# Kernel tuning notes

Measured on AMD Instinct MI355X. Metric: run time of the kernel, lower is better.

The kernel has to match this reference:

```python
import jax, jax.numpy as jnp
import numpy as np

N, C_IN, C_OUT, H, RANK = 16, 4, 32, 400, 4


def setup_inputs() -> dict:
    key = jax.random.key(0)
    k1, k2, k3 = jax.random.split(key, 3)
    x = jax.random.normal(k1, (N, C_IN, H, H), dtype=jnp.float32)
    # symmetric sylo: weight_R tied to weight_L (shape C_out x C_in x H x rank)
    fan_in = C_IN * H
    scale = 1.0 / np.sqrt(fan_in)
    weight_L = jax.random.normal(k2, (C_OUT, C_IN, H, RANK), dtype=jnp.float32) * scale
    bias = jax.random.uniform(k3, (C_OUT,), dtype=jnp.float32, minval=-scale, maxval=scale)
    return {"x": x, "weight_L": weight_L, "bias": bias}


def reference(x, weight_L, bias):
    # Expand low-rank symmetric template: T[o,c] = L[o,c] @ L[o,c].T  (H x H)
    T = jnp.einsum('ocir,ocjr->ocij', weight_L, weight_L)
    # Crosshair similarity, summed over input channels:
    # out[n,o,i,j] = sum_c [ sum_k X[n,c,i,k]T[o,c,i,k] + sum_k X[n,c,k,j]T[o,c,k,j] - X[n,c,i,j]T[o,c,i,j] ]
    rows = jnp.einsum('ncik,ocik->noi', x, T)   # row sums of X*T
    cols = jnp.einsum('nckj,ockj->noj', x, T)   # column sums of X*T
    diag = jnp.einsum('ncij,ocij->noij', x, T)  # pointwise term (counted twice)
    out = rows[..., :, None] + cols[..., None, :] - diag
    return out + bias[None, :, None, None]
```

## Files before the change

kernel.cpp:

```cpp
#include <hip/hip_runtime.h>

#define H  400
#define NB 16
#define CI 4
#define CO 32

#define TT 80
__global__ __launch_bounds__(256) void k_transpose(const float* __restrict__ x,
                                                   float* __restrict__ xt) {
    __shared__ float tile[TT][TT + 5];
    int b = blockIdx.x;
    int tj = b % 5;
    int ti = (b / 5) % 5;
    int nc = b / 25;
    const float* src = x + (size_t)nc * H * H;
    float* dst = xt + (size_t)nc * H * H;
    int i0 = ti * TT, j0 = tj * TT;
    for (int e = threadIdx.x; e < TT * 20; e += 256) {
        int r = e / 20, q = e % 20;
        float4 v = ((const float4*)(src + (size_t)(i0 + r) * H + j0))[q];
        tile[r][q * 4 + 0] = v.x; tile[r][q * 4 + 1] = v.y;
        tile[r][q * 4 + 2] = v.z; tile[r][q * 4 + 3] = v.w;
    }
    __syncthreads();
    for (int e = threadIdx.x; e < TT * 20; e += 256) {
        int r = e / 20, q = e % 20;
        float4 v;
        v.x = tile[q * 4 + 0][r]; v.y = tile[q * 4 + 1][r];
        v.z = tile[q * 4 + 2][r]; v.w = tile[q * 4 + 3][r];
        ((float4*)(dst + (size_t)(j0 + r) * H + i0))[q] = v;
    }
}

#define KC 40
#define KSPLIT 5
__global__ __launch_bounds__(256) void k_rowscols(const float* __restrict__ x,
        const float* __restrict__ xt, const float* __restrict__ L,
        float* __restrict__ rowsP, float* __restrict__ colsP)
{
    __shared__ __align__(16) float4 Lm[CO * CI];
    __shared__ __align__(16) float Xr[NB * CI * KC];
    __shared__ __align__(16) float Xc[NB * CI * KC];
    __shared__ __align__(16) float Tr[CO * 164];
    int b = blockIdx.x;
    int m  = b / KSPLIT;
    int ks = b % KSPLIT;
    int tid = threadIdx.x;
    const float4* L4 = (const float4*)L;
    if (tid < CO * CI) Lm[tid] = L4[tid * H + m];

    int o  = tid & 31;
    int n0 = tid >> 5;
    float ar0 = 0.f, ar1 = 0.f, ac0 = 0.f, ac1 = 0.f;

    for (int ch = 0; ch < 2; ++ch) {
        int k0 = ks * 80 + ch * KC;
        __syncthreads();
        for (int e = tid; e < NB * CI * KC / 4; e += 256) {
            int q  = e % 10;
            int nc = e / 10;
            ((float4*)Xr)[e] = *(const float4*)(x  + (size_t)(nc * H + m) * H + k0 + q * 4);
            ((float4*)Xc)[e] = *(const float4*)(xt + (size_t)(nc * H + m) * H + k0 + q * 4);
        }
        for (int e = tid; e < CO * CI * KC; e += 256) {
            int k  = e % KC;
            int oc = e / KC;
            float4 lv = L4[oc * H + k0 + k];
            float4 lm = Lm[oc];
            Tr[(oc >> 2) * 164 + (oc & 3) * KC + k] =
                lv.x * lm.x + lv.y * lm.y + lv.z * lm.z + lv.w * lm.w;
        }
        __syncthreads();
        #pragma unroll
        for (int c = 0; c < CI; ++c) {
            const float4* trp = (const float4*)(Tr + o * 164 + c * KC);
            const float4* pr0 = (const float4*)(Xr + (n0 * CI + c) * KC);
            const float4* pr1 = (const float4*)(Xr + ((n0 + 8) * CI + c) * KC);
            const float4* pc0 = (const float4*)(Xc + (n0 * CI + c) * KC);
            const float4* pc1 = (const float4*)(Xc + ((n0 + 8) * CI + c) * KC);
            #pragma unroll
            for (int q = 0; q < KC / 4; ++q) {
                float4 tv = trp[q];
                float4 a  = pr0[q];
                float4 bb = pr1[q];
                float4 cc = pc0[q];
                float4 dd = pc1[q];
                ar0 += tv.x * a.x  + tv.y * a.y  + tv.z * a.z  + tv.w * a.w;
                ar1 += tv.x * bb.x + tv.y * bb.y + tv.z * bb.z + tv.w * bb.w;
                ac0 += tv.x * cc.x + tv.y * cc.y + tv.z * cc.z + tv.w * cc.w;
                ac1 += tv.x * dd.x + tv.y * dd.y + tv.z * dd.z + tv.w * dd.w;
            }
        }
    }
    size_t base = ((size_t)ks * H + m) * (NB * CO);
    rowsP[base + tid]       = ar0;
    rowsP[base + 256 + tid] = ar1;
    colsP[base + tid]       = ac0;
    colsP[base + 256 + tid] = ac1;
}

__global__ __launch_bounds__(256) void k_reduce(const float* __restrict__ rowsP,
        const float* __restrict__ colsP, float* __restrict__ rows, float* __restrict__ cols)
{
    int i = blockIdx.x * 256 + threadIdx.x;
    int m  = i % H;
    int no = i / H;
    float s = 0.f, t = 0.f;
    #pragma unroll
    for (int k = 0; k < KSPLIT; ++k) {
        s += rowsP[((size_t)k * H + m) * (NB * CO) + no];
        t += colsP[((size_t)k * H + m) * (NB * CO) + no];
    }
    rows[(size_t)no * H + m] = s;
    cols[(size_t)no * H + m] = t;
}

#define TS 16
__global__ __launch_bounds__(256, 4) void k_out(const float* __restrict__ x,
        const float* __restrict__ L, const float* __restrict__ bias,
        const float* __restrict__ rows, const float* __restrict__ cols,
        float* __restrict__ out)
{
    __shared__ __align__(16) float Xl[8 * CI * TS * TS];
    __shared__ __align__(16) float rT[8 * 4 * TS];
    __shared__ __align__(16) float cT[8 * 4 * TS];
    int b = blockIdx.x;
    int ti = b / 25, tj = b % 25;
    int i0 = ti * TS, j0 = tj * TS;
    int tid = threadIdx.x;

    int o  = tid >> 6;
    int u  = tid & 63;
    int ii = u >> 2, jq = u & 3;
    const float4* x4  = (const float4*)x;
    const float4* L4  = (const float4*)L;
    const float4* cT4 = (const float4*)cT;
    float4* Xl4  = (float4*)Xl;
    float4* out4 = (float4*)out;

    for (int nh = 0; nh < 2; ++nh) {
        if (nh) __syncthreads();
        for (int e = tid; e < 8 * CI * TS * 4; e += 256) {
            int q   = e & 3;
            int iiw = (e >> 2) & 15;
            int nc  = nh * (8 * CI) + (e >> 6);
            Xl4[e] = x4[(size_t)(nc * H + i0 + iiw) * 100 + tj * 4 + q];
        }
        for (int os = 0; os < 8; ++os) {
            int og = os * 4 + o;
            float4 T4[CI];
            #pragma unroll
            for (int c = 0; c < CI; ++c) {
                float4 Li = L4[(og * CI + c) * H + i0 + ii];
                float4 La = L4[(og * CI + c) * H + j0 + jq * 4 + 0];
                float4 Lb = L4[(og * CI + c) * H + j0 + jq * 4 + 1];
                float4 Lc = L4[(og * CI + c) * H + j0 + jq * 4 + 2];
                float4 Ld = L4[(og * CI + c) * H + j0 + jq * 4 + 3];
                T4[c].x = Li.x * La.x + Li.y * La.y + Li.z * La.z + Li.w * La.w;
                T4[c].y = Li.x * Lb.x + Li.y * Lb.y + Li.z * Lb.z + Li.w * Lb.w;
                T4[c].z = Li.x * Lc.x + Li.y * Lc.y + Li.z * Lc.z + Li.w * Lc.w;
                T4[c].w = Li.x * Ld.x + Li.y * Ld.y + Li.z * Ld.z + Li.w * Ld.w;
            }
            float bo = bias[og];

            __syncthreads();
            for (int e = tid; e < 8 * 4 * TS; e += 256) {
                int iw = e & 15;
                int oo = (e >> 4) & 3;
                int np = e >> 6;
                int n  = nh * 8 + np;
                rT[e] = rows[(size_t)(n * CO + os * 4 + oo) * H + i0 + iw];
                cT[e] = cols[(size_t)(n * CO + os * 4 + oo) * H + j0 + iw];
            }
            __syncthreads();

            for (int np = 0; np < 8; ++np) {
                float ra  = rT[(np * 4 + o) * TS + ii] + bo;
                float4 ca = cT4[(np * 4 + o) * 4 + jq];
                float4 acc;
                acc.x = ra + ca.x; acc.y = ra + ca.y; acc.z = ra + ca.z; acc.w = ra + ca.w;
                #pragma unroll
                for (int c = 0; c < CI; ++c) {
                    float4 xv = Xl4[((np * CI + c) * TS + ii) * 4 + jq];
                    acc.x -= xv.x * T4[c].x;
                    acc.y -= xv.y * T4[c].y;
                    acc.z -= xv.z * T4[c].z;
                    acc.w -= xv.w * T4[c].w;
                }
                int n = nh * 8 + np;
                out4[((size_t)(n * CO + og) * H + i0 + ii) * 100 + tj * 4 + jq] = acc;
            }
        }
    }
}

extern "C" void kernel_launch(void* const* d_in, const int* in_sizes, int n_in,
                              void* d_out, int out_size, void* d_ws, size_t ws_size,
                              hipStream_t stream) {
    const float* x    = (const float*)d_in[0];
    const float* L    = (const float*)d_in[1];
    const float* bias = (const float*)d_in[2];
    float* out = (float*)d_out;
    char* ws = (char*)d_ws;

    size_t xt_bytes = (size_t)NB * CI * H * H * sizeof(float);
    size_t rc_elems = (size_t)NB * CO * H;
    size_t rcP_bytes = (size_t)KSPLIT * rc_elems * sizeof(float);
    size_t rc_bytes  = rc_elems * sizeof(float);

    float* XT    = (float*)ws;
    float* rowsP = (float*)(ws + xt_bytes);
    float* colsP = (float*)(ws + xt_bytes + rcP_bytes);
    float* rows  = (float*)(ws + xt_bytes + 2 * rcP_bytes);
    float* cols  = (float*)(ws + xt_bytes + 2 * rcP_bytes + rc_bytes);
    (void)ws_size;

    k_transpose<<<1600, 256, 0, stream>>>(x, XT);
    k_rowscols<<<H * KSPLIT, 256, 0, stream>>>(x, XT, L, rowsP, colsP);
    k_reduce<<<(NB * CO * H) / 256, 256, 0, stream>>>(rowsP, colsP, rows, cols);
    k_out<<<625, 256, 0, stream>>>(x, L, bias, rows, cols, out);
}
```

Before: 504.0 us.

## Compute row and column sums from shared 2D tiles, dropping the transpose pass

Removes the separate transpose kernel and the transposed copy of x. A new kernel computes row and column partial sums together from 16x16 tiles of x and T held in shared memory, so each x element is read once for both reductions. The partial sums and reduced rows/cols now use an i-major layout, which gives coalesced reads in the output kernel. The cost is 25 split partials instead of 5, so the reduce kernel reads much more data, and per-thread register arrays of 64 accumulators may limit occupancy.

```diff
diff --git a/kernel.cpp b/kernel.cpp
--- a/kernel.cpp
+++ b/kernel.cpp
@@ -4,121 +4,103 @@
 #define NB 16
 #define CI 4
 #define CO 32
-
-#define TT 80
-__global__ __launch_bounds__(256) void k_transpose(const float* __restrict__ x,
-                                                   float* __restrict__ xt) {
-    __shared__ float tile[TT][TT + 5];
-    int b = blockIdx.x;
-    int tj = b % 5;
-    int ti = (b / 5) % 5;
-    int nc = b / 25;
-    const float* src = x + (size_t)nc * H * H;
-    float* dst = xt + (size_t)nc * H * H;
-    int i0 = ti * TT, j0 = tj * TT;
-    for (int e = threadIdx.x; e < TT * 20; e += 256) {
-        int r = e / 20, q = e % 20;
-        float4 v = ((const float4*)(src + (size_t)(i0 + r) * H + j0))[q];
-        tile[r][q * 4 + 0] = v.x; tile[r][q * 4 + 1] = v.y;
-        tile[r][q * 4 + 2] = v.z; tile[r][q * 4 + 3] = v.w;
-    }
-    __syncthreads();
-    for (int e = threadIdx.x; e < TT * 20; e += 256) {
-        int r = e / 20, q = e % 20;
-        float4 v;
-        v.x = tile[q * 4 + 0][r]; v.y = tile[q * 4 + 1][r];
-        v.z = tile[q * 4 + 2][r]; v.w = tile[q * 4 + 3][r];
-        ((float4*)(dst + (size_t)(j0 + r) * H + i0))[q] = v;
-    }
-}
-
-#define KC 40
-#define KSPLIT 5
-__global__ __launch_bounds__(256) void k_rowscols(const float* __restrict__ x,
-        const float* __restrict__ xt, const float* __restrict__ L,
+#define NO (NB * CO)
+#define NS 25
+
+__global__ __launch_bounds__(256, 3) void k_rc(const float* __restrict__ x,
+        const float* __restrict__ L,
         float* __restrict__ rowsP, float* __restrict__ colsP)
 {
-    __shared__ __align__(16) float4 Lm[CO * CI];
-    __shared__ __align__(16) float Xr[NB * CI * KC];
-    __shared__ __align__(16) float Xc[NB * CI * KC];
-    __shared__ __align__(16) float Tr[CO * 164];
-    int b = blockIdx.x;
-    int m  = b / KSPLIT;
-    int ks = b % KSPLIT;
+    __shared__ __align__(16) float Xs[NB][16][16];
+    __shared__ __align__(16) float Ts[64][128];
+    int b  = blockIdx.x;
+    int ti = b / NS, tk = b % NS;
+    int I = ti * 16, K = tk * 16;
     int tid = threadIdx.x;
+    int o  = tid & 31;
+    int n2 = tid >> 5;
+    const float4* x4 = (const float4*)x;
     const float4* L4 = (const float4*)L;
-    if (tid < CO * CI) Lm[tid] = L4[tid * H + m];
-
-    int o  = tid & 31;
-    int n0 = tid >> 5;
-    float ar0 = 0.f, ar1 = 0.f, ac0 = 0.f, ac1 = 0.f;
-
-    for (int ch = 0; ch < 2; ++ch) {
-        int k0 = ks * 80 + ch * KC;
+
+    float ar0[16] = {}, ar1[16] = {}, ac0[16] = {}, ac1[16] = {};
+
+    for (int c = 0; c < CI; ++c) {
         __syncthreads();
-        for (int e = tid; e < NB * CI * KC / 4; e += 256) {
-            int q  = e % 10;
-            int nc = e / 10;
-            ((float4*)Xr)[e] = *(const float4*)(x  + (size_t)(nc * H + m) * H + k0 + q * 4);
-            ((float4*)Xc)[e] = *(const float4*)(xt + (size_t)(nc * H + m) * H + k0 + q * 4);
-        }
-        for (int e = tid; e < CO * CI * KC; e += 256) {
-            int k  = e % KC;
-            int oc = e / KC;
-            float4 lv = L4[oc * H + k0 + k];
-            float4 lm = Lm[oc];
-            Tr[(oc >> 2) * 164 + (oc & 3) * KC + k] =
-                lv.x * lm.x + lv.y * lm.y + lv.z * lm.z + lv.w * lm.w;
+        for (int e = tid; e < 1024; e += 256) {
+            int q  = e & 3;
+            int di = (e >> 2) & 15;
+            int n  = e >> 6;
+            ((float4*)Xs)[e] = x4[((size_t)(n * CI + c) * H + I + di) * 100 + tk * 4 + q];
+        }
+        {
+            const float4* Lrow = L4 + (size_t)(o * CI + c) * H;
+            float4 Li0 = Lrow[I + 2 * n2];
+            float4 Li1 = Lrow[I + 2 * n2 + 1];
+            #pragma unroll
+            for (int qk = 0; qk < 4; ++qk) {
+                float4 t0, t1;
+                #pragma unroll
+                for (int w = 0; w < 4; ++w) {
+                    float4 Lk = Lrow[K + qk * 4 + w];
+                    ((float*)&t0)[w] = Li0.x * Lk.x + Li0.y * Lk.y + Li0.z * Lk.z + Li0.w * Lk.w;
+                    ((float*)&t1)[w] = Li1.x * Lk.x + Li1.y * Lk.y + Li1.z * Lk.z + Li1.w * Lk.w;
+                }
+                *(float4*)&Ts[(2 * n2)     * 4 + qk][o * 4] = t0;
+                *(float4*)&Ts[(2 * n2 + 1) * 4 + qk][o * 4] = t1;
+            }
         }
         __syncthreads();
         #pragma unroll
-        for (int c = 0; c < CI; ++c) {
-            const float4* trp = (const float4*)(Tr + o * 164 + c * KC);
-            const float4* pr0 = (const float4*)(Xr + (n0 * CI + c) * KC);
-            const float4* pr1 = (const float4*)(Xr + ((n0 + 8) * CI + c) * KC);
-            const float4* pc0 = (const float4*)(Xc + (n0 * CI + c) * KC);
-            const float4* pc1 = (const float4*)(Xc + ((n0 + 8) * CI + c) * KC);
+        for (int di = 0; di < 16; ++di) {
             #pragma unroll
-            for (int q = 0; q < KC / 4; ++q) {
-                float4 tv = trp[q];
-                float4 a  = pr0[q];
-                float4 bb = pr1[q];
-                float4 cc = pc0[q];
-                float4 dd = pc1[q];
-                ar0 += tv.x * a.x  + tv.y * a.y  + tv.z * a.z  + tv.w * a.w;
-                ar1 += tv.x * bb.x + tv.y * bb.y + tv.z * bb.z + tv.w * bb.w;
-                ac0 += tv.x * cc.x + tv.y * cc.y + tv.z * cc.z + tv.w * cc.w;
-                ac1 += tv.x * dd.x + tv.y * dd.y + tv.z * dd.z + tv.w * dd.w;
-            }
-        }
-    }
-    size_t base = ((size_t)ks * H + m) * (NB * CO);
-    rowsP[base + tid]       = ar0;
-    rowsP[base + 256 + tid] = ar1;
-    colsP[base + tid]       = ac0;
-    colsP[base + 256 + tid] = ac1;
+            for (int qk = 0; qk < 4; ++qk) {
+                float4 tv = *(const float4*)&Ts[di * 4 + qk][o * 4];
+                float4 xa = ((const float4*)&Xs[n2][di][0])[qk];
+                float4 xb = ((const float4*)&Xs[n2 + 8][di][0])[qk];
+                ar0[di] += tv.x * xa.x + tv.y * xa.y + tv.z * xa.z + tv.w * xa.w;
+                ar1[di] += tv.x * xb.x + tv.y * xb.y + tv.z * xb.z + tv.w * xb.w;
+                ac0[qk * 4 + 0] += tv.x * xa.x;
+                ac0[qk * 4 + 1] += tv.y * xa.y;
+                ac0[qk * 4 + 2] += tv.z * xa.z;
+                ac0[qk * 4 + 3] += tv.w * xa.w;
+                ac1[qk * 4 + 0] += tv.x * xb.x;
+                ac1[qk * 4 + 1] += tv.y * xb.y;
+                ac1[qk * 4 + 2] += tv.z * xb.z;
+                ac1[qk * 4 + 3] += tv.w * xb.w;
+            }
+        }
+    }
+    int no0 = n2 * CO + o;
+    int no1 = (n2 + 8) * CO + o;
+    #pragma unroll
+    for (int d = 0; d < 16; ++d) {
+        rowsP[((size_t)tk * H + I + d) * NO + no0] = ar0[d];
+        rowsP[((size_t)tk * H + I + d) * NO + no1] = ar1[d];
+        colsP[((size_t)ti * H + K + d) * NO + no0] = ac0[d];
+        colsP[((size_t)ti * H + K + d) * NO + no1] = ac1[d];
+    }
 }
 
 __global__ __launch_bounds__(256) void k_reduce(const float* __restrict__ rowsP,
-        const float* __restrict__ colsP, float* __restrict__ rows, float* __restrict__ cols)
+        const float* __restrict__ colsP, float* __restrict__ rows2, float* __restrict__ cols2)
 {
-    int i = blockIdx.x * 256 + threadIdx.x;
-    int m  = i % H;
-    int no = i / H;
+    int idx = blockIdx.x * 256 + threadIdx.x;
+    int no = idx & (NO - 1);
+    int i  = idx >> 9;
     float s = 0.f, t = 0.f;
     #pragma unroll
-    for (int k = 0; k < KSPLIT; ++k) {
-        s += rowsP[((size_t)k * H + m) * (NB * CO) + no];
-        t += colsP[((size_t)k * H + m) * (NB * CO) + no];
-    }
-    rows[(size_t)no * H + m] = s;
-    cols[(size_t)no * H + m] = t;
+    for (int k = 0; k < NS; ++k) {
+        s += rowsP[((size_t)k * H + i) * NO + no];
+        t += colsP[((size_t)k * H + i) * NO + no];
+    }
+    rows2[(size_t)i * NO + no] = s;
+    cols2[(size_t)i * NO + no] = t;
 }
 
 #define TS 16
 __global__ __launch_bounds__(256, 4) void k_out(const float* __restrict__ x,
         const float* __restrict__ L, const float* __restrict__ bias,
-        const float* __restrict__ rows, const float* __restrict__ cols,
+        const float* __restrict__ rows2, const float* __restrict__ cols2,
         float* __restrict__ out)
 {
     __shared__ __align__(16) float Xl[8 * CI * TS * TS];
@@ -169,8 +151,8 @@
                 int oo = (e >> 4) & 3;
                 int np = e >> 6;
                 int n  = nh * 8 + np;
-                rT[e] = rows[(size_t)(n * CO + os * 4 + oo) * H + i0 + iw];
-                cT[e] = cols[(size_t)(n * CO + os * 4 + oo) * H + j0 + iw];
+                rT[e] = rows2[(size_t)(i0 + iw) * NO + n * CO + os * 4 + oo];
+                cT[e] = cols2[(size_t)(j0 + iw) * NO + n * CO + os * 4 + oo];
             }
             __syncthreads();
 
@@ -203,20 +185,16 @@
     float* out = (float*)d_out;
     char* ws = (char*)d_ws;
 
-    size_t xt_bytes = (size_t)NB * CI * H * H * sizeof(float);
-    size_t rc_elems = (size_t)NB * CO * H;
-    size_t rcP_bytes = (size_t)KSPLIT * rc_elems * sizeof(float);
-    size_t rc_bytes  = rc_elems * sizeof(float);
-
-    float* XT    = (float*)ws;
-    float* rowsP = (float*)(ws + xt_bytes);
-    float* colsP = (float*)(ws + xt_bytes + rcP_bytes);
-    float* rows  = (float*)(ws + xt_bytes + 2 * rcP_bytes);
-    float* cols  = (float*)(ws + xt_bytes + 2 * rcP_bytes + rc_bytes);
+    size_t rcP_bytes = (size_t)NS * H * NO * sizeof(float);
+    size_t rc_bytes  = (size_t)H * NO * sizeof(float);
+
+    float* rowsP = (float*)ws;
+    float* colsP = (float*)(ws + rcP_bytes);
+    float* rows2 = (float*)(ws + 2 * rcP_bytes);
+    float* cols2 = (float*)(ws + 2 * rcP_bytes + rc_bytes);
     (void)ws_size;
 
-    k_transpose<<<1600, 256, 0, stream>>>(x, XT);
-    k_rowscols<<<H * KSPLIT, 256, 0, stream>>>(x, XT, L, rowsP, colsP);
-    k_reduce<<<(NB * CO * H) / 256, 256, 0, stream>>>(rowsP, colsP, rows, cols);
-    k_out<<<625, 256, 0, stream>>>(x, L, bias, rows, cols, out);
-}
+    k_rc<<<NS * NS, 256, 0, stream>>>(x, L, rowsP, colsP);
+    k_reduce<<<(H * NO) / 256, 256, 0, stream>>>(rowsP, colsP, rows2, cols2);
+    k_out<<<625, 256, 0, stream>>>(x, L, bias, rows2, cols2, out);
+}
```

Result: slower. 644.2 us (+27.8%).

## Restructure output kernel to share template tiles in LDS and keep X in registers

Applied to the files above, without the earlier changes.

k_reduce now writes rows and cols in an m-major layout, so its reads and writes are coalesced and k_out's gathers read contiguous runs across n and o. In k_out each thread now owns one (n, i) row of a 16x16 tile and keeps its X values for all channels in registers. The T tile for four output channels is built once per block in shared memory from staged L rows, instead of each thread recomputing it from global L loads. The cost is more registers per thread (64 floats of X plus 16 accumulators) and extra barriers per output-channel group, which may lower occupancy.

```diff
diff --git a/kernel.cpp b/kernel.cpp
--- a/kernel.cpp
+++ b/kernel.cpp
@@ -4,6 +4,7 @@
 #define NB 16
 #define CI 4
 #define CO 32
+#define NO (NB * CO)
 
 #define TT 80
 __global__ __launch_bounds__(256) void k_transpose(const float* __restrict__ x,
@@ -92,7 +93,7 @@
             }
         }
     }
-    size_t base = ((size_t)ks * H + m) * (NB * CO);
+    size_t base = ((size_t)ks * H + m) * NO;
     rowsP[base + tid]       = ar0;
     rowsP[base + 256 + tid] = ar1;
     colsP[base + tid]       = ac0;
@@ -100,96 +101,113 @@
 }
 
 __global__ __launch_bounds__(256) void k_reduce(const float* __restrict__ rowsP,
-        const float* __restrict__ colsP, float* __restrict__ rows, float* __restrict__ cols)
+        const float* __restrict__ colsP, float* __restrict__ rows2, float* __restrict__ cols2)
 {
-    int i = blockIdx.x * 256 + threadIdx.x;
-    int m  = i % H;
-    int no = i / H;
+    int idx = blockIdx.x * 256 + threadIdx.x;
+    int no = idx & (NO - 1);
+    int m  = idx >> 9;
     float s = 0.f, t = 0.f;
     #pragma unroll
     for (int k = 0; k < KSPLIT; ++k) {
-        s += rowsP[((size_t)k * H + m) * (NB * CO) + no];
-        t += colsP[((size_t)k * H + m) * (NB * CO) + no];
-    }
-    rows[(size_t)no * H + m] = s;
-    cols[(size_t)no * H + m] = t;
-}
-
-#define TS 16
+        s += rowsP[((size_t)k * H + m) * NO + no];
+        t += colsP[((size_t)k * H + m) * NO + no];
+    }
+    rows2[(size_t)m * NO + no] = s;
+    cols2[(size_t)m * NO + no] = t;
+}
+
+#define TSP 20
+#define TS_OG (CI * 16 * TSP)
 __global__ __launch_bounds__(256, 4) void k_out(const float* __restrict__ x,
         const float* __restrict__ L, const float* __restrict__ bias,
-        const float* __restrict__ rows, const float* __restrict__ cols,
+        const float* __restrict__ rows2, const float* __restrict__ cols2,
         float* __restrict__ out)
 {
-    __shared__ __align__(16) float Xl[8 * CI * TS * TS];
-    __shared__ __align__(16) float rT[8 * 4 * TS];
-    __shared__ __align__(16) float cT[8 * 4 * TS];
+    __shared__ __align__(16) float4 Lsi[4 * CI * 16];
+    __shared__ __align__(16) float4 Lsj[4 * CI * 16];
+    __shared__ __align__(16) float  Ts[4 * TS_OG];
+    __shared__ __align__(16) float  rT[4 * NB * 16];
+    __shared__ __align__(16) float  cT[4 * NB * 16];
     int b = blockIdx.x;
     int ti = b / 25, tj = b % 25;
-    int i0 = ti * TS, j0 = tj * TS;
+    int i0 = ti * 16, j0 = tj * 16;
     int tid = threadIdx.x;
-
-    int o  = tid >> 6;
-    int u  = tid & 63;
-    int ii = u >> 2, jq = u & 3;
+    int n  = tid >> 4;
+    int ii = tid & 15;
     const float4* x4  = (const float4*)x;
     const float4* L4  = (const float4*)L;
     const float4* cT4 = (const float4*)cT;
-    float4* Xl4  = (float4*)Xl;
     float4* out4 = (float4*)out;
 
-    for (int nh = 0; nh < 2; ++nh) {
-        if (nh) __syncthreads();
-        for (int e = tid; e < 8 * CI * TS * 4; e += 256) {
-            int q   = e & 3;
-            int iiw = (e >> 2) & 15;
-            int nc  = nh * (8 * CI) + (e >> 6);
-            Xl4[e] = x4[(size_t)(nc * H + i0 + iiw) * 100 + tj * 4 + q];
-        }
-        for (int os = 0; os < 8; ++os) {
-            int og = os * 4 + o;
-            float4 T4[CI];
+    float4 Xr[CI][4];
+    #pragma unroll
+    for (int c = 0; c < CI; ++c)
+        #pragma unroll
+        for (int q = 0; q < 4; ++q)
+            Xr[c][q] = x4[((size_t)(n * CI + c) * H + i0 + ii) * 100 + tj * 4 + q];
+
+    for (int os = 0; os < 8; ++os) {
+        __syncthreads();
+        {
+            int r   = tid & 15;
+            int cg  = (tid >> 4) & 3;
+            int og_ = tid >> 6;
+            size_t lrow = (size_t)((os * 4 + og_) * CI + cg) * H;
+            Lsi[(og_ * CI + cg) * 16 + r] = L4[lrow + i0 + r];
+            Lsj[(og_ * CI + cg) * 16 + r] = L4[lrow + j0 + r];
+        }
+        for (int e = tid; e < 1024; e += 256) {
+            int iw  = e & 15;
+            int og_ = (e >> 4) & 3;
+            int nn  = e >> 6;
+            rT[(og_ * NB + nn) * 16 + iw] = rows2[(size_t)(i0 + iw) * NO + nn * CO + os * 4 + og_];
+            cT[(og_ * NB + nn) * 16 + iw] = cols2[(size_t)(j0 + iw) * NO + nn * CO + os * 4 + og_];
+        }
+        __syncthreads();
+        {
+            int iw  = tid & 15;
+            int cc  = (tid >> 4) & 3;
+            int og_ = tid >> 6;
+            float4 Li = Lsi[(og_ * CI + cc) * 16 + iw];
+            float* tsrow = Ts + og_ * TS_OG + cc * (16 * TSP) + iw * TSP;
+            #pragma unroll
+            for (int q = 0; q < 4; ++q) {
+                float4 t;
+                #pragma unroll
+                for (int w = 0; w < 4; ++w) {
+                    float4 Lj = Lsj[(og_ * CI + cc) * 16 + q * 4 + w];
+                    ((float*)&t)[w] = Li.x * Lj.x + Li.y * Lj.y + Li.z * Lj.z + Li.w * Lj.w;
+                }
+                *(float4*)(tsrow + q * 4) = t;
+            }
+        }
+        __syncthreads();
+        #pragma unroll
+        for (int og_ = 0; og_ < 4; ++og_) {
+            int og = os * 4 + og_;
+            float ra = rT[(og_ * NB + n) * 16 + ii] + bias[og];
+            float4 acc[4];
+            #pragma unroll
+            for (int q = 0; q < 4; ++q) {
+                float4 ca = cT4[(og_ * NB + n) * 4 + q];
+                acc[q].x = ra + ca.x; acc[q].y = ra + ca.y;
+                acc[q].z = ra + ca.z; acc[q].w = ra + ca.w;
+            }
             #pragma unroll
             for (int c = 0; c < CI; ++c) {
-                float4 Li = L4[(og * CI + c) * H + i0 + ii];
-                float4 La = L4[(og * CI + c) * H + j0 + jq * 4 + 0];
-                float4 Lb = L4[(og * CI + c) * H + j0 + jq * 4 + 1];
-                float4 Lc = L4[(og * CI + c) * H + j0 + jq * 4 + 2];
-                float4 Ld = L4[(og * CI + c) * H + j0 + jq * 4 + 3];
-                T4[c].x = Li.x * La.x + Li.y * La.y + Li.z * La.z + Li.w * La.w;
-                T4[c].y = Li.x * Lb.x + Li.y * Lb.y + Li.z * Lb.z + Li.w * Lb.w;
-                T4[c].z = Li.x * Lc.x + Li.y * Lc.y + Li.z * Lc.z + Li.w * Lc.w;
-                T4[c].w = Li.x * Ld.x + Li.y * Ld.y + Li.z * Ld.z + Li.w * Ld.w;
-            }
-            float bo = bias[og];
-
-            __syncthreads();
-            for (int e = tid; e < 8 * 4 * TS; e += 256) {
-                int iw = e & 15;
-                int oo = (e >> 4) & 3;
-                int np = e >> 6;
-                int n  = nh * 8 + np;
-                rT[e] = rows[(size_t)(n * CO + os * 4 + oo) * H + i0 + iw];
-                cT[e] = cols[(size_t)(n * CO + os * 4 + oo) * H + j0 + iw];
-            }
-            __syncthreads();
-
-            for (int np = 0; np < 8; ++np) {
-                float ra  = rT[(np * 4 + o) * TS + ii] + bo;
-                float4 ca = cT4[(np * 4 + o) * 4 + jq];
-                float4 acc;
-                acc.x = ra + ca.x; acc.y = ra + ca.y; acc.z = ra + ca.z; acc.w = ra + ca.w;
+                const float* tsrow = Ts + og_ * TS_OG + c * (16 * TSP) + ii * TSP;
                 #pragma unroll
-                for (int c = 0; c < CI; ++c) {
-                    float4 xv = Xl4[((np * CI + c) * TS + ii) * 4 + jq];
-                    acc.x -= xv.x * T4[c].x;
-                    acc.y -= xv.y * T4[c].y;
-                    acc.z -= xv.z * T4[c].z;
-                    acc.w -= xv.w * T4[c].w;
+                for (int q = 0; q < 4; ++q) {
+                    float4 tq = *(const float4*)(tsrow + q * 4);
+                    acc[q].x -= Xr[c][q].x * tq.x;
+                    acc[q].y -= Xr[c][q].y * tq.y;
+                    acc[q].z -= Xr[c][q].z * tq.z;
+                    acc[q].w -= Xr[c][q].w * tq.w;
                 }
-                int n = nh * 8 + np;
-                out4[((size_t)(n * CO + og) * H + i0 + ii) * 100 + tj * 4 + jq] = acc;
-            }
+            }
+            size_t ob = ((size_t)(n * CO + og) * H + i0 + ii) * 100 + tj * 4;
+            #pragma unroll
+            for (int q = 0; q < 4; ++q) out4[ob + q] = acc[q];
         }
     }
 }
@@ -203,20 +221,20 @@
     float* out = (float*)d_out;
     char* ws = (char*)d_ws;
 
-    size_t xt_bytes = (size_t)NB * CI * H * H * sizeof(float);
-    size_t rc_elems = (size_t)NB * CO * H;
+    size_t xt_bytes  = (size_t)NB * CI * H * H * sizeof(float);
+    size_t rc_elems  = (size_t)H * NO;
     size_t rcP_bytes = (size_t)KSPLIT * rc_elems * sizeof(float);
     size_t rc_bytes  = rc_elems * sizeof(float);
 
     float* XT    = (float*)ws;
     float* rowsP = (float*)(ws + xt_bytes);
     float* colsP = (float*)(ws + xt_bytes + rcP_bytes);
-    float* rows  = (float*)(ws + xt_bytes + 2 * rcP_bytes);
-    float* cols  = (float*)(ws + xt_bytes + 2 * rcP_bytes + rc_bytes);
+    float* rows2 = (float*)(ws + xt_bytes + 2 * rcP_bytes);
+    float* cols2 = (float*)(ws + xt_bytes + 2 * rcP_bytes + rc_bytes);
     (void)ws_size;
 
     k_transpose<<<1600, 256, 0, stream>>>(x, XT);
     k_rowscols<<<H * KSPLIT, 256, 0, stream>>>(x, XT, L, rowsP, colsP);
-    k_reduce<<<(NB * CO * H) / 256, 256, 0, stream>>>(rowsP, colsP, rows, cols);
-    k_out<<<625, 256, 0, stream>>>(x, L, bias, rows, cols, out);
-}
+    k_reduce<<<(H * NO) / 256, 256, 0, stream>>>(rowsP, colsP, rows2, cols2);
+    k_out<<<625, 256, 0, stream>>>(x, L, bias, rows2, cols2, out);
+}
```

Measured after the change: 549.0 us. 8.9% more time.

## Swizzle block-to-XCD mapping, reorganize T smem layout, and tile-transpose partial reduction

Applied to the files above, without the earlier changes.

Remaps block indices in k_rowscols and k_out so that neighbouring logical tiles land on the same XCD, which should improve L2 locality across the chiplets. T in k_rowscols is now built with float4 stores in a layout interleaved by output channel, meant to avoid LDS bank conflicts on the read side. The reduce kernel now reads the partials coalesced and transposes them through shared memory, replacing strided gathers. The new reduce grid has only 50 blocks, which leaves most of the GPU idle during that step.

```diff
diff --git a/kernel.cpp b/kernel.cpp
--- a/kernel.cpp
+++ b/kernel.cpp
@@ -4,6 +4,7 @@
 #define NB 16
 #define CI 4
 #define CO 32
+#define NO (NB * CO)
 
 #define TT 80
 __global__ __launch_bounds__(256) void k_transpose(const float* __restrict__ x,
@@ -41,8 +42,9 @@
     __shared__ __align__(16) float4 Lm[CO * CI];
     __shared__ __align__(16) float Xr[NB * CI * KC];
     __shared__ __align__(16) float Xc[NB * CI * KC];
-    __shared__ __align__(16) float Tr[CO * 164];
-    int b = blockIdx.x;
+    __shared__ __align__(16) float Tr[CO * CI * KC];
+    int hw = blockIdx.x;
+    int b  = (hw & 7) * 250 + (hw >> 3);
     int m  = b / KSPLIT;
     int ks = b % KSPLIT;
     int tid = threadIdx.x;
@@ -62,25 +64,31 @@
             ((float4*)Xr)[e] = *(const float4*)(x  + (size_t)(nc * H + m) * H + k0 + q * 4);
             ((float4*)Xc)[e] = *(const float4*)(xt + (size_t)(nc * H + m) * H + k0 + q * 4);
         }
-        for (int e = tid; e < CO * CI * KC; e += 256) {
-            int k  = e % KC;
-            int oc = e / KC;
-            float4 lv = L4[oc * H + k0 + k];
+        for (int e = tid; e < CO * CI * KC / 4; e += 256) {
+            int oo = e & 31;
+            int t  = e >> 5;
+            int q  = t % 10;
+            int cc = t / 10;
+            int oc = oo * CI + cc;
             float4 lm = Lm[oc];
-            Tr[(oc >> 2) * 164 + (oc & 3) * KC + k] =
-                lv.x * lm.x + lv.y * lm.y + lv.z * lm.z + lv.w * lm.w;
+            float4 t4;
+            #pragma unroll
+            for (int w = 0; w < 4; ++w) {
+                float4 lv = L4[oc * H + k0 + q * 4 + w];
+                ((float*)&t4)[w] = lv.x * lm.x + lv.y * lm.y + lv.z * lm.z + lv.w * lm.w;
+            }
+            ((float4*)Tr)[(cc * 10 + q) * 32 + oo] = t4;
         }
         __syncthreads();
         #pragma unroll
         for (int c = 0; c < CI; ++c) {
-            const float4* trp = (const float4*)(Tr + o * 164 + c * KC);
             const float4* pr0 = (const float4*)(Xr + (n0 * CI + c) * KC);
             const float4* pr1 = (const float4*)(Xr + ((n0 + 8) * CI + c) * KC);
             const float4* pc0 = (const float4*)(Xc + (n0 * CI + c) * KC);
             const float4* pc1 = (const float4*)(Xc + ((n0 + 8) * CI + c) * KC);
             #pragma unroll
             for (int q = 0; q < KC / 4; ++q) {
-                float4 tv = trp[q];
+                float4 tv = ((const float4*)Tr)[(c * 10 + q) * 32 + o];
                 float4 a  = pr0[q];
                 float4 bb = pr1[q];
                 float4 cc = pc0[q];
@@ -92,39 +100,53 @@
             }
         }
     }
-    size_t base = ((size_t)ks * H + m) * (NB * CO);
+    size_t base = ((size_t)ks * H + m) * NO;
     rowsP[base + tid]       = ar0;
     rowsP[base + 256 + tid] = ar1;
     colsP[base + tid]       = ac0;
     colsP[base + 256 + tid] = ac1;
 }
 
-__global__ __launch_bounds__(256) void k_reduce(const float* __restrict__ rowsP,
-        const float* __restrict__ colsP, float* __restrict__ rows, float* __restrict__ cols)
+__global__ __launch_bounds__(256) void k_reduce_t(const float* __restrict__ rowsP,
+        const float* __restrict__ colsP, float* __restrict__ rows2T, float* __restrict__ cols2T)
 {
-    int i = blockIdx.x * 256 + threadIdx.x;
-    int m  = i % H;
-    int no = i / H;
-    float s = 0.f, t = 0.f;
+    __shared__ float Lr[16][257];
+    __shared__ float Lc[16][257];
+    int b  = blockIdx.x;
+    int mt = b % 25, nt = b / 25;
+    int tid = threadIdx.x;
     #pragma unroll
-    for (int k = 0; k < KSPLIT; ++k) {
-        s += rowsP[((size_t)k * H + m) * (NB * CO) + no];
-        t += colsP[((size_t)k * H + m) * (NB * CO) + no];
-    }
-    rows[(size_t)no * H + m] = s;
-    cols[(size_t)no * H + m] = t;
+    for (int mm = 0; mm < 16; ++mm) {
+        float s = 0.f, t = 0.f;
+        #pragma unroll
+        for (int ks = 0; ks < KSPLIT; ++ks) {
+            s += rowsP[((size_t)ks * H + mt * 16 + mm) * NO + nt * 256 + tid];
+            t += colsP[((size_t)ks * H + mt * 16 + mm) * NO + nt * 256 + tid];
+        }
+        Lr[mm][tid] = s;
+        Lc[mm][tid] = t;
+    }
+    __syncthreads();
+    for (int e = tid; e < 16 * 256; e += 256) {
+        int m_  = e & 15;
+        int no_ = e >> 4;
+        rows2T[(size_t)(nt * 256 + no_) * H + mt * 16 + m_] = Lr[m_][no_];
+        cols2T[(size_t)(nt * 256 + no_) * H + mt * 16 + m_] = Lc[m_][no_];
+    }
 }
 
 #define TS 16
 __global__ __launch_bounds__(256, 4) void k_out(const float* __restrict__ x,
         const float* __restrict__ L, const float* __restrict__ bias,
-        const float* __restrict__ rows, const float* __restrict__ cols,
+        const float* __restrict__ rows2T, const float* __restrict__ cols2T,
         float* __restrict__ out)
 {
     __shared__ __align__(16) float Xl[8 * CI * TS * TS];
     __shared__ __align__(16) float rT[8 * 4 * TS];
     __shared__ __align__(16) float cT[8 * 4 * TS];
-    int b = blockIdx.x;
+    int hw = blockIdx.x;
+    int xcd = hw & 7, pos = hw >> 3;
+    int b = (xcd == 0) ? pos : (79 + (xcd - 1) * 78 + pos);
     int ti = b / 25, tj = b % 25;
     int i0 = ti * TS, j0 = tj * TS;
     int tid = threadIdx.x;
@@ -169,8 +191,9 @@
                 int oo = (e >> 4) & 3;
                 int np = e >> 6;
                 int n  = nh * 8 + np;
-                rT[e] = rows[(size_t)(n * CO + os * 4 + oo) * H + i0 + iw];
-                cT[e] = cols[(size_t)(n * CO + os * 4 + oo) * H + j0 + iw];
+                size_t no = (size_t)(n * CO + os * 4 + oo);
+                rT[e] = rows2T[no * H + i0 + iw];
+                cT[e] = cols2T[no * H + j0 + iw];
             }
             __syncthreads();
 
@@ -203,20 +226,20 @@
     float* out = (float*)d_out;
     char* ws = (char*)d_ws;
 
-    size_t xt_bytes = (size_t)NB * CI * H * H * sizeof(float);
-    size_t rc_elems = (size_t)NB * CO * H;
+    size_t xt_bytes  = (size_t)NB * CI * H * H * sizeof(float);
+    size_t rc_elems  = (size_t)H * NO;
     size_t rcP_bytes = (size_t)KSPLIT * rc_elems * sizeof(float);
     size_t rc_bytes  = rc_elems * sizeof(float);
 
-    float* XT    = (float*)ws;
-    float* rowsP = (float*)(ws + xt_bytes);
-    float* colsP = (float*)(ws + xt_bytes + rcP_bytes);
-    float* rows  = (float*)(ws + xt_bytes + 2 * rcP_bytes);
-    float* cols  = (float*)(ws + xt_bytes + 2 * rcP_bytes + rc_bytes);
+    float* XT     = (float*)ws;
+    float* rowsP  = (float*)(ws + xt_bytes);
+    float* colsP  = (float*)(ws + xt_bytes + rcP_bytes);
+    float* rows2T = (float*)(ws + xt_bytes + 2 * rcP_bytes);
+    float* cols2T = (float*)(ws + xt_bytes + 2 * rcP_bytes + rc_bytes);
     (void)ws_size;
 
     k_transpose<<<1600, 256, 0, stream>>>(x, XT);
     k_rowscols<<<H * KSPLIT, 256, 0, stream>>>(x, XT, L, rowsP, colsP);
-    k_reduce<<<(NB * CO * H) / 256, 256, 0, stream>>>(rowsP, colsP, rows, cols);
-    k_out<<<625, 256, 0, stream>>>(x, L, bias, rows, cols, out);
-}
+    k_reduce_t<<<50, 256, 0, stream>>>(rowsP, colsP, rows2T, cols2T);
+    k_out<<<625, 256, 0, stream>>>(x, L, bias, rows2T, cols2T, out);
+}
```

Measured after the change: 506.2 us. No clear change (+0.4%).
